# Kernel optimization log

Measured on AMD Instinct MI355X. Metric: run time of the kernel, lower is better.

## Reference

```python
import jax, jax.numpy as jnp
import numpy as np

NUM_AREAS = 4
NUM_TICKS = 4
AREA_N = 2048          # neurons per area
N = NUM_AREAS * AREA_N # total neurons = 8192
D_IN = 1024
N_CLASSES = 1024
BATCH = 512
THRESHOLD = 0.05


def setup_inputs() -> dict:
    key = jax.random.key(0)
    ks = jax.random.split(key, 9)
    x = jax.random.normal(ks[0], (BATCH, D_IN), jnp.float32)
    Rw = jax.random.normal(ks[1], (NUM_AREAS, AREA_N, D_IN), jnp.float32) * 0.02
    rb = jax.random.normal(ks[2], (NUM_AREAS, AREA_N), jnp.float32) * 0.02
    W_blocks = jax.random.normal(ks[3], (NUM_AREAS, NUM_AREAS, AREA_N, AREA_N), jnp.float32) * 0.02
    # bias only on diagonal blocks (in_area == out_area), else zeros, as in torch code
    b_full = jax.random.normal(ks[4], (NUM_AREAS, AREA_N), jnp.float32) * 0.02
    b_blocks = jnp.zeros((NUM_AREAS, NUM_AREAS, AREA_N), jnp.float32)
    b_blocks = b_blocks.at[jnp.arange(NUM_AREAS), jnp.arange(NUM_AREAS)].set(b_full)
    # mask init: 0.5 on diagonal blocks, 0.05 off-diagonal
    eye = jnp.eye(NUM_AREAS, dtype=jnp.float32)
    mask = (0.05 + 0.45 * eye)[:, :, None, None] * jnp.ones((NUM_AREAS, NUM_AREAS, AREA_N, AREA_N), jnp.float32)
    Ow = jax.random.normal(ks[5], (N_CLASSES, N), jnp.float32) * 0.02
    Ob = jax.random.normal(ks[6], (N_CLASSES,), jnp.float32) * 0.02
    # KMeans-like neuron partition: random permutation split into equal areas
    area_idx = jax.random.permutation(ks[7], N).reshape(NUM_AREAS, AREA_N).astype(jnp.int64)
    return {"x": x, "Rw": Rw, "rb": rb, "W_blocks": W_blocks, "b_blocks": b_blocks,
            "mask": mask, "Ow": Ow, "Ob": Ob, "area_idx": area_idx}


def reference(x, Rw, rb, W_blocks, b_blocks, mask, Ow, Ob, area_idx):
    # Initial per-area encoding: Z[a] = tanh(x @ Rw[a].T + rb[a]) -> [A, B, n]
    Z = jnp.tanh(jnp.einsum('bd,and->abn', x, Rw) + rb[:, None, :])
    history = [Z]
    # Effective masked weights (clamp mask to [0,1])
    Weff = W_blocks * jnp.clip(mask, 0.0, 1.0)  # [A_out, A_in, n_out, n_in]
    for _ in range(NUM_TICKS):
        # data-dependent skip: connection fires only if mean|Z_in| > threshold
        gate = (jnp.mean(jnp.abs(Z), axis=(1, 2)) > THRESHOLD).astype(Z.dtype)  # [A_in]
        Zg = Z * gate[:, None, None]
        Z_next = jnp.einsum('ibm,oinm->obn', Zg, Weff)
        Z_next = Z_next + jnp.einsum('i,oin->on', gate, b_blocks)[:, None, :]
        Z = jnp.tanh(Z_next)
        history.append(Z)
    B = x.shape[0]
    # Scatter per-area activations back to flat neuron order
    Zperm = jnp.transpose(Z, (1, 0, 2)).reshape(B, N)  # columns ordered as area_idx.reshape(-1)
    Z_flat = jnp.zeros((B, N), x.dtype).at[:, area_idx.reshape(-1)].set(Zperm)
    logits = Z_flat @ Ow.T + Ob
    return logits, jnp.stack(history)  # history: [T+1, A, B, n]
```

## Files before the change

kernel.cpp:

```cpp
#include <hip/hip_runtime.h>
#include <stdint.h>

typedef unsigned short u16;
typedef float floatx4 __attribute__((ext_vector_type(4)));
typedef __bf16 bf16x8 __attribute__((ext_vector_type(8)));
typedef float f32x4v __attribute__((ext_vector_type(4)));
typedef unsigned u32x4v __attribute__((ext_vector_type(4)));

#define NUM_AREAS 4
#define AN 2048
#define NTOT 8192
#define BATCH 512
#define DIN 1024
#define NCLS 1024
#define THRESHOLD 0.05f
#define BAN (BATCH * AN)

__device__ __forceinline__ u16 f2bf(float f) {
    union { float f; unsigned u; } v; v.f = f;
    unsigned r = v.u + 0x7fffu + ((v.u >> 16) & 1u);
    return (u16)(r >> 16);
}

__device__ __forceinline__ void load_lds16(const u16* g, u16* l) {
    __builtin_amdgcn_global_load_lds((const __attribute__((address_space(1))) void*)g,
                                     (__attribute__((address_space(3))) void*)l,
                                     16, 0, 0);
}

__device__ __forceinline__ void gemm_db(const u16* __restrict__ A, int lda,
                                        const u16* __restrict__ Bm, int ldb,
                                        int klen, u16* sA, u16* sB,
                                        floatx4 acc[4][4]) {
    const int tid = threadIdx.x;
    const int t8 = tid * 8;
    const int lane = tid & 63;
    const int quad = lane >> 4;
    const int l15 = lane & 15;
    const int wm = ((tid >> 7) & 1) * 64;
    const int wn = ((tid >> 6) & 1) * 64;
    const int r0 = t8 >> 5;
    const int kk = t8 & 31;
    const int nst = klen >> 5;

    auto stage = [&](int buf, int k0) {
        const int bo = buf << 12;
        load_lds16(A + (size_t)r0 * lda + (k0 + kk), sA + bo + t8);
        load_lds16(Bm + (size_t)r0 * ldb + (k0 + kk), sB + bo + t8);
        load_lds16(A + (size_t)(r0 + 64) * lda + (k0 + kk), sA + bo + 2048 + t8);
        load_lds16(Bm + (size_t)(r0 + 64) * ldb + (k0 + kk), sB + bo + 2048 + t8);
    };

    stage(0, 0);
    __syncthreads();
    int buf = 0;
    for (int t = 0; t < nst; ++t) {
        const int bo = buf << 12;
        bf16x8 av[4], bv[4];
#pragma unroll
        for (int i = 0; i < 4; ++i)
            av[i] = *(const bf16x8*)(sA + bo + (wm + i * 16 + l15) * 32 + quad * 8);
#pragma unroll
        for (int i = 0; i < 4; ++i)
            bv[i] = *(const bf16x8*)(sB + bo + (wn + i * 16 + l15) * 32 + quad * 8);
        if (t + 1 < nst) stage(buf ^ 1, (t + 1) << 5);
#pragma unroll
        for (int mt = 0; mt < 4; ++mt)
#pragma unroll
            for (int nt = 0; nt < 4; ++nt)
                acc[mt][nt] = __builtin_amdgcn_mfma_f32_16x16x32_bf16(av[mt], bv[nt], acc[mt][nt], 0, 0, 0);
        __syncthreads();
        buf ^= 1;
    }
}

__global__ void k_init(const float* __restrict__ Ob, float* __restrict__ out,
                       float* __restrict__ gacc) {
    const int i = blockIdx.x * 256 + threadIdx.x;
    if (i < BATCH * NCLS) out[i] = Ob[i & (NCLS - 1)];
    if (i < 32) gacc[i] = 0.f;
}

__global__ void k_cvt(const float* __restrict__ src, u16* __restrict__ dst, int n8) {
    const int i = blockIdx.x * 256 + threadIdx.x;
    if (i >= n8) return;
    const float4 x0 = ((const float4*)src)[2 * i];
    const float4 x1 = ((const float4*)src)[2 * i + 1];
    uint4 o;
    o.x = (unsigned)f2bf(x0.x) | ((unsigned)f2bf(x0.y) << 16);
    o.y = (unsigned)f2bf(x0.z) | ((unsigned)f2bf(x0.w) << 16);
    o.z = (unsigned)f2bf(x1.x) | ((unsigned)f2bf(x1.y) << 16);
    o.w = (unsigned)f2bf(x1.z) | ((unsigned)f2bf(x1.w) << 16);
    ((uint4*)dst)[i] = o;
}

__global__ void k_weff(const float* __restrict__ W, const float* __restrict__ mask,
                       u16* __restrict__ dst) {
    const int i = blockIdx.x * 256 + threadIdx.x;
    const f32x4v* wp = (const f32x4v*)W + (size_t)4 * i;
    const f32x4v* mp = (const f32x4v*)mask + (size_t)4 * i;
    f32x4v w0 = wp[0], w1 = wp[1], w2 = wp[2], w3 = wp[3];
    f32x4v m0 = mp[0], m1 = mp[1], m2 = mp[2], m3 = mp[3];
    asm volatile("" :: "v"(w0), "v"(w1), "v"(w2), "v"(w3),
                       "v"(m0), "v"(m1), "v"(m2), "v"(m3));
    #define CL(m) fminf(fmaxf((m), 0.f), 1.f)
    #define PK(wa, ma, wb, mb) ((unsigned)f2bf((wa) * CL(ma)) | ((unsigned)f2bf((wb) * CL(mb)) << 16))
    u32x4v o0, o1;
    o0[0] = PK(w0[0], m0[0], w0[1], m0[1]);
    o0[1] = PK(w0[2], m0[2], w0[3], m0[3]);
    o0[2] = PK(w1[0], m1[0], w1[1], m1[1]);
    o0[3] = PK(w1[2], m1[2], w1[3], m1[3]);
    o1[0] = PK(w2[0], m2[0], w2[1], m2[1]);
    o1[1] = PK(w2[2], m2[2], w2[3], m2[3]);
    o1[2] = PK(w3[0], m3[0], w3[1], m3[1]);
    o1[3] = PK(w3[2], m3[2], w3[3], m3[3]);
    #undef PK
    #undef CL
    u32x4v* dp = (u32x4v*)dst + (size_t)2 * i;
    dp[0] = o0;
    dp[1] = o1;
}

__global__ void k_enc(const u16* __restrict__ xbf, const u16* __restrict__ rwbf,
                      const float* __restrict__ rb, float* __restrict__ hist0,
                      u16* __restrict__ z0, float* __restrict__ gacc) {
    __shared__ __align__(16) u16 smemA[8192];
    __shared__ __align__(16) u16 smemB[8192];
    __shared__ float red[4];
    floatx4 acc[4][4] = {};
    const int mb = blockIdx.y, nb = blockIdx.x;
    gemm_db(xbf + (size_t)mb * 128 * DIN, DIN,
            rwbf + (size_t)nb * 128 * DIN, DIN, DIN, smemA, smemB, acc);
    const int tid = threadIdx.x, lane = tid & 63, quad = lane >> 4, l15 = lane & 15;
    const int wm = ((tid >> 7) & 1) * 64, wn = ((tid >> 6) & 1) * 64;
    const int cbase = nb * 128;
    const int area = cbase >> 11;
    float asum = 0.f;
#pragma unroll
    for (int nt = 0; nt < 4; ++nt) {
        const int col = cbase + wn + nt * 16 + l15;
        const int n = col & (AN - 1);
        const float bias = rb[col];
#pragma unroll
        for (int mt = 0; mt < 4; ++mt) {
#pragma unroll
            for (int r = 0; r < 4; ++r) {
                const int row = mb * 128 + wm + mt * 16 + quad * 4 + r;
                const float z = tanhf(acc[mt][nt][r] + bias);
                asum += fabsf(z);
                const size_t idx = (size_t)area * BAN + (size_t)row * AN + n;
                hist0[idx] = z;
                z0[idx] = f2bf(z);
            }
        }
    }
    for (int off = 32; off > 0; off >>= 1) asum += __shfl_down(asum, off, 64);
    if (lane == 0) red[tid >> 6] = asum;
    __syncthreads();
    if (tid == 0) atomicAdd(&gacc[area], red[0] + red[1] + red[2] + red[3]);
}

__global__ __launch_bounds__(512, 2)
void k_tick_mm(const u16* __restrict__ zprev, const u16* __restrict__ weff,
               const float* __restrict__ gin, float* __restrict__ zacc) {
    __shared__ __align__(16) u16 sA[3][8192];
    __shared__ __align__(16) u16 sB[3][8192];
    const int nb = blockIdx.x, mb = blockIdx.y, i = blockIdx.z;
    const float thr = THRESHOLD * (float)BAN;
    if (!(gin[i] > thr)) return;

    const int o = nb >> 3;
    const int nbase = (nb & 7) * 256;
    const int tid = threadIdx.x;
    const int lane = tid & 63, quad = lane >> 4, l15 = lane & 15;
    const int w = tid >> 6;
    const int wm = (w >> 2) * 128;
    const int wn = (w & 3) * 64;

    const u16* Abase = zprev + (size_t)i * BAN + (size_t)mb * 256 * AN;
    const u16* Bbase = weff + ((size_t)(o * 4 + i) * AN + nbase) * AN;
    const int r0 = tid >> 2;
    const int kq = (tid & 3) * 8;
    const u16* pA0 = Abase + (size_t)r0 * AN + kq;
    const u16* pA1 = Abase + (size_t)(r0 + 128) * AN + kq;
    const u16* pB0 = Bbase + (size_t)r0 * AN + kq;
    const u16* pB1 = Bbase + (size_t)(r0 + 128) * AN + kq;
    u16* dA0 = &sA[0][tid * 8];
    u16* dA1 = &sA[0][tid * 8 + 4096];
    u16* dB0 = &sB[0][tid * 8];
    u16* dB1 = &sB[0][tid * 8 + 4096];

    auto stage = [&](int slot, int kt) {
        const int ko = kt * 32;
        const int so = slot * 8192;
        load_lds16(pA0 + ko, dA0 + so);
        load_lds16(pA1 + ko, dA1 + so);
        load_lds16(pB0 + ko, dB0 + so);
        load_lds16(pB1 + ko, dB1 + so);
    };

    floatx4 acc[8][4] = {};

    stage(0, 0);
    stage(1, 1);
    asm volatile("s_waitcnt vmcnt(4)" ::: "memory");
    __builtin_amdgcn_s_barrier();

    const int NKT = AN / 32;
    for (int kt = 0; kt < NKT; ++kt) {
        if (kt + 2 < NKT) stage((kt + 2) % 3, kt + 2);
        const int sl = kt % 3;
        bf16x8 av[8], bv[4];
#pragma unroll
        for (int mt = 0; mt < 8; ++mt)
            av[mt] = *(const bf16x8*)(&sA[sl][(wm + mt * 16 + l15) * 32 + quad * 8]);
#pragma unroll
        for (int nt = 0; nt < 4; ++nt)
            bv[nt] = *(const bf16x8*)(&sB[sl][(wn + nt * 16 + l15) * 32 + quad * 8]);
        __builtin_amdgcn_s_setprio(1);
#pragma unroll
        for (int mt = 0; mt < 8; ++mt)
#pragma unroll
            for (int nt = 0; nt < 4; ++nt)
                acc[mt][nt] = __builtin_amdgcn_mfma_f32_16x16x32_bf16(av[mt], bv[nt], acc[mt][nt], 0, 0, 0);
        __builtin_amdgcn_s_setprio(0);
        if (kt < NKT - 2) {
            asm volatile("s_waitcnt vmcnt(4)" ::: "memory");
        } else {
            asm volatile("s_waitcnt vmcnt(0)" ::: "memory");
        }
        __builtin_amdgcn_s_barrier();
    }

    float* __restrict__ dst = zacc + ((size_t)i * 4 + o) * BAN;
#pragma unroll
    for (int mt = 0; mt < 8; ++mt) {
#pragma unroll
        for (int nt = 0; nt < 4; ++nt) {
            const int n = nbase + wn + nt * 16 + l15;
#pragma unroll
            for (int r = 0; r < 4; ++r) {
                const int row = mb * 256 + wm + mt * 16 + quad * 4 + r;
                dst[(size_t)row * AN + n] = acc[mt][nt][r];
            }
        }
    }
}

__global__ void k_tick_ep(const float* __restrict__ zacc, const float* __restrict__ bblk,
                          const float* __restrict__ gin, float* __restrict__ hist,
                          u16* __restrict__ zcur, float* __restrict__ gout) {
    __shared__ float red[4];
    const int tid = threadIdx.x;
    const int t8 = (blockIdx.x * 256 + tid) * 8;
    const int o = t8 >> 20;
    const int n = t8 & (AN - 1);
    const int io = t8 & (BAN - 1);
    const float thr = THRESHOLD * (float)BAN;
    float s[8] = {0.f, 0.f, 0.f, 0.f, 0.f, 0.f, 0.f, 0.f};
#pragma unroll
    for (int i = 0; i < 4; ++i) {
        if (!(gin[i] > thr)) continue;
        const float4* p = (const float4*)(zacc + ((size_t)i * 4 + o) * BAN + io);
        const float4 x0 = p[0], x1 = p[1];
        const float4* bb = (const float4*)(bblk + (size_t)(o * 4 + i) * AN + n);
        const float4 b0 = bb[0], b1 = bb[1];
        s[0] += x0.x + b0.x; s[1] += x0.y + b0.y; s[2] += x0.z + b0.z; s[3] += x0.w + b0.w;
        s[4] += x1.x + b1.x; s[5] += x1.y + b1.y; s[6] += x1.z + b1.z; s[7] += x1.w + b1.w;
    }
    float4 h0, h1;
    uint4 zb;
    const float z0 = tanhf(s[0]), z1 = tanhf(s[1]), z2 = tanhf(s[2]), z3 = tanhf(s[3]);
    const float z4 = tanhf(s[4]), z5 = tanhf(s[5]), z6 = tanhf(s[6]), z7 = tanhf(s[7]);
    float asum = fabsf(z0) + fabsf(z1) + fabsf(z2) + fabsf(z3)
               + fabsf(z4) + fabsf(z5) + fabsf(z6) + fabsf(z7);
    h0.x = z0; h0.y = z1; h0.z = z2; h0.w = z3;
    h1.x = z4; h1.y = z5; h1.z = z6; h1.w = z7;
    zb.x = (unsigned)f2bf(z0) | ((unsigned)f2bf(z1) << 16);
    zb.y = (unsigned)f2bf(z2) | ((unsigned)f2bf(z3) << 16);
    zb.z = (unsigned)f2bf(z4) | ((unsigned)f2bf(z5) << 16);
    zb.w = (unsigned)f2bf(z6) | ((unsigned)f2bf(z7) << 16);
    ((float4*)(hist + t8))[0] = h0;
    ((float4*)(hist + t8))[1] = h1;
    *((uint4*)(zcur + t8)) = zb;
    for (int off = 32; off > 0; off >>= 1) asum += __shfl_down(asum, off, 64);
    if ((tid & 63) == 0) red[tid >> 6] = asum;
    __syncthreads();
    if (tid == 0) atomicAdd(&gout[o], red[0] + red[1] + red[2] + red[3]);
}

__global__ void k_scatter(const u16* __restrict__ z4, const int* __restrict__ aidx,
                          u16* __restrict__ zflat) {
    const int i = blockIdx.x * 256 + threadIdx.x;
    const int n = i & (AN - 1);
    const int bb = (i >> 11) & (BATCH - 1);
    const int a = i >> 20;
    const int j = aidx[a * AN + n];
    zflat[(size_t)bb * NTOT + j] = z4[i];
}

__global__ void k_out(const u16* __restrict__ zflat, const u16* __restrict__ owbf,
                      float* __restrict__ out) {
    __shared__ __align__(16) u16 smemA[8192];
    __shared__ __align__(16) u16 smemB[8192];
    floatx4 acc[4][4] = {};
    const int nb = blockIdx.x, mb = blockIdx.y, ks = blockIdx.z;
    gemm_db(zflat + (size_t)mb * 128 * NTOT + ks * 1024, NTOT,
            owbf + (size_t)nb * 128 * NTOT + ks * 1024, NTOT, 1024,
            smemA, smemB, acc);
    const int tid = threadIdx.x, lane = tid & 63, quad = lane >> 4, l15 = lane & 15;
    const int wm = ((tid >> 7) & 1) * 64, wn = ((tid >> 6) & 1) * 64;
#pragma unroll
    for (int mt = 0; mt < 4; ++mt)
#pragma unroll
        for (int nt = 0; nt < 4; ++nt)
#pragma unroll
            for (int r = 0; r < 4; ++r) {
                const int row = mb * 128 + wm + mt * 16 + quad * 4 + r;
                const int col = nb * 128 + wn + nt * 16 + l15;
                atomicAdd(&out[(size_t)row * NCLS + col], acc[mt][nt][r]);
            }
}

extern "C" void kernel_launch(void* const* d_in, const int* in_sizes, int n_in,
                              void* d_out, int out_size, void* d_ws, size_t ws_size,
                              hipStream_t stream) {
    (void)in_sizes; (void)n_in; (void)out_size; (void)ws_size;
    const float* x    = (const float*)d_in[0];
    const float* Rw   = (const float*)d_in[1];
    const float* rb   = (const float*)d_in[2];
    const float* Wb   = (const float*)d_in[3];
    const float* bblk = (const float*)d_in[4];
    const float* mask = (const float*)d_in[5];
    const float* Ow   = (const float*)d_in[6];
    const float* Ob   = (const float*)d_in[7];
    const int*   aidx = (const int*)d_in[8];

    float* out  = (float*)d_out;
    float* hist = out + (size_t)BATCH * NCLS;

    char* ws = (char*)d_ws;
    size_t off = 0;
    auto alloc = [&](size_t bytes) -> char* {
        char* p = ws + off;
        off += (bytes + 255) & ~(size_t)255;
        return p;
    };
    u16* weffbf = (u16*)alloc((size_t)16 * AN * AN * 2);
    float* zacc = (float*)alloc((size_t)16 * BAN * 4);
    u16* rwbf  = (u16*)zacc;
    u16* owbf  = (u16*)((char*)zacc + ((size_t)16 << 20));
    u16* zflat = (u16*)((char*)zacc + ((size_t)32 << 20));
    u16* xbf    = (u16*)alloc((size_t)BATCH * DIN * 2);
    u16* zb0    = (u16*)alloc((size_t)NUM_AREAS * BAN * 2);
    u16* zb1    = (u16*)alloc((size_t)NUM_AREAS * BAN * 2);
    float* gacc = (float*)alloc(32 * 4);
    u16* zb[2]  = { zb0, zb1 };

    k_init<<<(BATCH * NCLS + 255) / 256, 256, 0, stream>>>(Ob, out, gacc);
    k_cvt<<<(BATCH * DIN / 8) / 256, 256, 0, stream>>>(x, xbf, BATCH * DIN / 8);
    k_cvt<<<(NTOT * DIN / 8) / 256, 256, 0, stream>>>(Rw, rwbf, NTOT * DIN / 8);
    k_weff<<<16384, 256, 0, stream>>>(Wb, mask, weffbf);

    dim3 g1(64, 4);
    k_enc<<<g1, 256, 0, stream>>>(xbf, rwbf, rb, hist, zb[0], gacc);
    dim3 gmm(32, 2, 4);
    for (int t = 1; t <= 4; ++t) {
        k_tick_mm<<<gmm, 512, 0, stream>>>(zb[(t + 1) & 1], weffbf,
                                           gacc + (t - 1) * 4, zacc);
        k_tick_ep<<<2048, 256, 0, stream>>>(zacc, bblk, gacc + (t - 1) * 4,
                                            hist + (size_t)t * NUM_AREAS * BAN,
                                            zb[t & 1], gacc + t * 4);
    }
    k_cvt<<<(NCLS * NTOT / 8) / 256, 256, 0, stream>>>(Ow, owbf, NCLS * NTOT / 8);
    k_scatter<<<(NUM_AREAS * BAN) / 256, 256, 0, stream>>>(zb[0], aidx, zflat);
    k_out<<<dim3(8, 4, 8), 256, 0, stream>>>(zflat, owbf, out);
}
```

Baseline: 1.128 ms.

## Pre-tile bf16 activations and weights into contiguous k-slab layout for tick GEMM

Stores the bf16 Z activations and masked weights in a tiled layout where each 256x32 k-slab is contiguous. The tick GEMM can then fetch each slab with fully contiguous 16-byte global-to-LDS loads instead of row-strided ones. The weight conversion kernel is rewritten to emit the tiled layout, and the encoder, epilogue and scatter kernels are updated to write or read the new indexing. The risk is that the weight conversion and the encoder stores now scatter more.

```diff
diff --git a/kernel.cpp b/kernel.cpp
--- a/kernel.cpp
+++ b/kernel.cpp
@@ -15,6 +15,10 @@
 #define NCLS 1024
 #define THRESHOLD 0.05f
 #define BAN (BATCH * AN)
+
+__device__ __forceinline__ size_t zpk(int a, int b, int n) {
+    return ((((size_t)a * 2 + (b >> 8)) * 64 + (n >> 5)) << 13) | ((b & 255) << 5) | (n & 31);
+}
 
 __device__ __forceinline__ u16 f2bf(float f) {
     union { float f; unsigned u; } v; v.f = f;
@@ -94,31 +98,36 @@
     ((uint4*)dst)[i] = o;
 }
 
-__global__ void k_weff(const float* __restrict__ W, const float* __restrict__ mask,
-                       u16* __restrict__ dst) {
-    const int i = blockIdx.x * 256 + threadIdx.x;
-    const f32x4v* wp = (const f32x4v*)W + (size_t)4 * i;
-    const f32x4v* mp = (const f32x4v*)mask + (size_t)4 * i;
-    f32x4v w0 = wp[0], w1 = wp[1], w2 = wp[2], w3 = wp[3];
-    f32x4v m0 = mp[0], m1 = mp[1], m2 = mp[2], m3 = mp[3];
-    asm volatile("" :: "v"(w0), "v"(w1), "v"(w2), "v"(w3),
-                       "v"(m0), "v"(m1), "v"(m2), "v"(m3));
-    #define CL(m) fminf(fmaxf((m), 0.f), 1.f)
-    #define PK(wa, ma, wb, mb) ((unsigned)f2bf((wa) * CL(ma)) | ((unsigned)f2bf((wb) * CL(mb)) << 16))
-    u32x4v o0, o1;
-    o0[0] = PK(w0[0], m0[0], w0[1], m0[1]);
-    o0[1] = PK(w0[2], m0[2], w0[3], m0[3]);
-    o0[2] = PK(w1[0], m1[0], w1[1], m1[1]);
-    o0[3] = PK(w1[2], m1[2], w1[3], m1[3]);
-    o1[0] = PK(w2[0], m2[0], w2[1], m2[1]);
-    o1[1] = PK(w2[2], m2[2], w2[3], m2[3]);
-    o1[2] = PK(w3[0], m3[0], w3[1], m3[1]);
-    o1[3] = PK(w3[2], m3[2], w3[3], m3[3]);
-    #undef PK
-    #undef CL
-    u32x4v* dp = (u32x4v*)dst + (size_t)2 * i;
-    dp[0] = o0;
-    dp[1] = o1;
+#define CLM(m) fminf(fmaxf((m), 0.f), 1.f)
+#define PKW(wa, ma, wb, mb) ((unsigned)f2bf((wa) * CLM(ma)) | ((unsigned)f2bf((wb) * CLM(mb)) << 16))
+
+__global__ void k_weffp(const float* __restrict__ W, const float* __restrict__ mask,
+                        u16* __restrict__ dst) {
+    const int ktg = blockIdx.x, nb = blockIdx.y, o4i = blockIdx.z;
+    const int t = threadIdx.x;
+    u16* dt = dst + (((size_t)o4i * 8 + nb) * 64 + (size_t)ktg * 4) * 8192;
+    const float* Wb = W + ((size_t)o4i * 2048 + nb * 256) * 2048;
+    const float* Mb = mask + ((size_t)o4i * 2048 + nb * 256) * 2048;
+    const int kk = (t & 3) * 8;
+    const int rb = t >> 2;
+#pragma unroll
+    for (int s = 0; s < 4; ++s) {
+        const int k0 = (ktg * 4 + s) * 32 + kk;
+#pragma unroll
+        for (int v = 0; v < 4; ++v) {
+            const int r = v * 64 + rb;
+            const float4* wp = (const float4*)(Wb + (size_t)r * 2048 + k0);
+            const float4* mp = (const float4*)(Mb + (size_t)r * 2048 + k0);
+            const float4 w0 = wp[0], w1 = wp[1];
+            const float4 m0 = mp[0], m1 = mp[1];
+            uint4 ov;
+            ov.x = PKW(w0.x, m0.x, w0.y, m0.y);
+            ov.y = PKW(w0.z, m0.z, w0.w, m0.w);
+            ov.z = PKW(w1.x, m1.x, w1.y, m1.y);
+            ov.w = PKW(w1.z, m1.z, w1.w, m1.w);
+            *(uint4*)(dt + (size_t)s * 8192 + (size_t)v * 2048 + t * 8) = ov;
+        }
+    }
 }
 
 __global__ void k_enc(const u16* __restrict__ xbf, const u16* __restrict__ rwbf,
@@ -148,9 +157,8 @@
                 const int row = mb * 128 + wm + mt * 16 + quad * 4 + r;
                 const float z = tanhf(acc[mt][nt][r] + bias);
                 asum += fabsf(z);
-                const size_t idx = (size_t)area * BAN + (size_t)row * AN + n;
-                hist0[idx] = z;
-                z0[idx] = f2bf(z);
+                hist0[(size_t)area * BAN + (size_t)row * AN + n] = z;
+                z0[zpk(area, row, n)] = f2bf(z);
             }
         }
     }
@@ -170,33 +178,26 @@
     if (!(gin[i] > thr)) return;
 
     const int o = nb >> 3;
-    const int nbase = (nb & 7) * 256;
+    const int nb8 = nb & 7;
+    const int nbase = nb8 * 256;
     const int tid = threadIdx.x;
     const int lane = tid & 63, quad = lane >> 4, l15 = lane & 15;
     const int w = tid >> 6;
     const int wm = (w >> 2) * 128;
     const int wn = (w & 3) * 64;
 
-    const u16* Abase = zprev + (size_t)i * BAN + (size_t)mb * 256 * AN;
-    const u16* Bbase = weff + ((size_t)(o * 4 + i) * AN + nbase) * AN;
-    const int r0 = tid >> 2;
-    const int kq = (tid & 3) * 8;
-    const u16* pA0 = Abase + (size_t)r0 * AN + kq;
-    const u16* pA1 = Abase + (size_t)(r0 + 128) * AN + kq;
-    const u16* pB0 = Bbase + (size_t)r0 * AN + kq;
-    const u16* pB1 = Bbase + (size_t)(r0 + 128) * AN + kq;
-    u16* dA0 = &sA[0][tid * 8];
-    u16* dA1 = &sA[0][tid * 8 + 4096];
-    u16* dB0 = &sB[0][tid * 8];
-    u16* dB1 = &sB[0][tid * 8 + 4096];
+    const u16* Ap = zprev + ((size_t)(i * 2 + mb) * 64) * 8192 + tid * 8;
+    const u16* Bp = weff + ((size_t)((o * 4 + i) * 8 + nb8) * 64) * 8192 + tid * 8;
+    u16* dA = &sA[0][tid * 8];
+    u16* dB = &sB[0][tid * 8];
 
     auto stage = [&](int slot, int kt) {
-        const int ko = kt * 32;
+        const size_t go = (size_t)kt * 8192;
         const int so = slot * 8192;
-        load_lds16(pA0 + ko, dA0 + so);
-        load_lds16(pA1 + ko, dA1 + so);
-        load_lds16(pB0 + ko, dB0 + so);
-        load_lds16(pB1 + ko, dB1 + so);
+        load_lds16(Ap + go, dA + so);
+        load_lds16(Ap + go + 4096, dA + so + 4096);
+        load_lds16(Bp + go, dB + so);
+        load_lds16(Bp + go + 4096, dB + so + 4096);
     };
 
     floatx4 acc[8][4] = {};
@@ -256,6 +257,7 @@
     const int o = t8 >> 20;
     const int n = t8 & (AN - 1);
     const int io = t8 & (BAN - 1);
+    const int b = io >> 11;
     const float thr = THRESHOLD * (float)BAN;
     float s[8] = {0.f, 0.f, 0.f, 0.f, 0.f, 0.f, 0.f, 0.f};
 #pragma unroll
@@ -282,7 +284,7 @@
     zb.w = (unsigned)f2bf(z6) | ((unsigned)f2bf(z7) << 16);
     ((float4*)(hist + t8))[0] = h0;
     ((float4*)(hist + t8))[1] = h1;
-    *((uint4*)(zcur + t8)) = zb;
+    *((uint4*)(zcur + zpk(o, b, n))) = zb;
     for (int off = 32; off > 0; off >>= 1) asum += __shfl_down(asum, off, 64);
     if ((tid & 63) == 0) red[tid >> 6] = asum;
     __syncthreads();
@@ -292,11 +294,14 @@
 __global__ void k_scatter(const u16* __restrict__ z4, const int* __restrict__ aidx,
                           u16* __restrict__ zflat) {
     const int i = blockIdx.x * 256 + threadIdx.x;
-    const int n = i & (AN - 1);
-    const int bb = (i >> 11) & (BATCH - 1);
     const int a = i >> 20;
+    const int rest = i & (BAN - 1);
+    const int tile = rest >> 13;
+    const int within = rest & 8191;
+    const int b = ((tile >> 6) << 8) | (within >> 5);
+    const int n = ((tile & 63) << 5) | (within & 31);
     const int j = aidx[a * AN + n];
-    zflat[(size_t)bb * NTOT + j] = z4[i];
+    zflat[(size_t)b * NTOT + j] = z4[i];
 }
 
 __global__ void k_out(const u16* __restrict__ zflat, const u16* __restrict__ owbf,
@@ -360,7 +365,7 @@
     k_init<<<(BATCH * NCLS + 255) / 256, 256, 0, stream>>>(Ob, out, gacc);
     k_cvt<<<(BATCH * DIN / 8) / 256, 256, 0, stream>>>(x, xbf, BATCH * DIN / 8);
     k_cvt<<<(NTOT * DIN / 8) / 256, 256, 0, stream>>>(Rw, rwbf, NTOT * DIN / 8);
-    k_weff<<<16384, 256, 0, stream>>>(Wb, mask, weffbf);
+    k_weffp<<<dim3(16, 8, 16), 256, 0, stream>>>(Wb, mask, weffbf);
 
     dim3 g1(64, 4);
     k_enc<<<g1, 256, 0, stream>>>(xbf, rwbf, rb, hist, zb[0], gacc);
```

Result: no change. 1.135 ms (+0.6%).
